# Performance work log

Measured on AMD Instinct MI355X. Metric: run time of the kernel, lower is better.

The kernel has to match this reference:

```python
import jax, jax.numpy as jnp
import numpy as np

N_BITS = 64
N_GROUPS = 8
P = N_BITS // N_GROUPS          # bits per group = 8
MAX_TABLE = 2 ** (P + N_GROUPS - 1)  # 32768, largest group-mapper table
BATCH = 524288


def setup_inputs() -> dict:
    key = jax.random.key(0)
    k1, k2, k3 = jax.random.split(key, 3)
    # input bit patterns [B, n_bits], values in {0,1}
    bits = jax.random.randint(k1, (BATCH, N_BITS), 0, 2, dtype=jnp.int32)
    # group mapper RAM tables, padded to max address space; table for group g
    # only uses the first 2^(P+g) addresses (addresses never exceed that range)
    group_tables = jax.random.uniform(k2, (N_GROUPS, P, MAX_TABLE), dtype=jnp.float32)
    # carry detector tables: one 1-neuron table per group boundary, binary outputs
    carry_tables = jax.random.randint(k3, (N_GROUPS - 1, 2 ** P), 0, 2, dtype=jnp.int32)
    return {"bits": bits, "group_tables": group_tables, "carry_tables": carry_tables}


def reference(bits, group_tables, carry_tables):
    B = bits.shape[0]
    gb = bits.reshape(B, N_GROUPS, P)                       # [B, G, P]
    # MSB-first address per group (matches reversed-bit enumeration in source)
    w = (2 ** (P - 1 - jnp.arange(P))).astype(jnp.int32)    # [P]
    gaddr = jnp.einsum('bgp,p->bg', gb, w)                  # [B, G] int32
    # carry detector g reads the raw bits of group g (independent of other carries)
    carries = carry_tables[jnp.arange(N_GROUPS - 1)[None, :],
                           gaddr[:, :N_GROUPS - 1]]          # [B, G-1] in {0,1}
    outs = []
    for g in range(N_GROUPS):  # small fixed loop over structurally distinct tables
        addr = gaddr[:, g]
        if g > 0:
            # mapper input = cat([group_bits, carries[0:g]]); group bits are high bits
            cw = (2 ** (g - 1 - jnp.arange(g))).astype(jnp.int32)
            addr = addr * (2 ** g) + carries[:, :g] @ cw
        # gather each neuron's table entry at this address -> [B, P]
        outs.append(jnp.take(group_tables[g], addr, axis=1).T)
    return jnp.stack(outs, axis=1).reshape(B, N_BITS)
```

## Files before the change

### kernel.cpp

```cpp
#include <hip/hip_runtime.h>

#define N_BITS   64
#define N_GROUPS 8
#define PDIM     8
#define MAX_TABLE 32768
#define BATCH    524288

__global__ __launch_bounds__(256) void comp_mapper_kernel(
    const int*   __restrict__ bits,
    const float* __restrict__ gt,
    const int*   __restrict__ ct,
    float*       __restrict__ out)
{
    const int tid = blockIdx.x * blockDim.x + threadIdx.x;
    const int g   = tid & 7;

    const int4* bp = reinterpret_cast<const int4*>(bits) + (size_t)tid * 2;
    int4 x = bp[0];
    int4 y = bp[1];

    int gaddr = (x.x << 7) | (x.y << 6) | (x.z << 5) | (x.w << 4)
              | (y.x << 3) | (y.y << 2) | (y.z << 1) |  y.w;

    int carry = 0;
    if (g < 7) carry = ct[g * 256 + gaddr];

    unsigned long long m = __ballot(carry);
    const int lane = threadIdx.x & 63;
    const int base = lane & ~7;
    unsigned f = (unsigned)((m >> base) & 0xFFull);
    unsigned v = (__brev(f) >> 24) >> (8 - g);

    const int addr = (gaddr << g) | (int)v;

    const float* t = gt + (size_t)g * (PDIM * MAX_TABLE) + addr;
    float4 o0, o1;
    o0.x = t[0 * MAX_TABLE];
    o0.y = t[1 * MAX_TABLE];
    o0.z = t[2 * MAX_TABLE];
    o0.w = t[3 * MAX_TABLE];
    o1.x = t[4 * MAX_TABLE];
    o1.y = t[5 * MAX_TABLE];
    o1.z = t[6 * MAX_TABLE];
    o1.w = t[7 * MAX_TABLE];

    float4* op = reinterpret_cast<float4*>(out) + (size_t)tid * 2;
    op[0] = o0;
    op[1] = o1;
}

extern "C" void kernel_launch(void* const* d_in, const int* in_sizes, int n_in,
                              void* d_out, int out_size, void* d_ws, size_t ws_size,
                              hipStream_t stream) {
    const int*   bits = (const int*)  d_in[0];
    const float* gt   = (const float*)d_in[1];
    const int*   ct   = (const int*)  d_in[2];
    float*       out  = (float*)      d_out;

    const int total_threads = BATCH * N_GROUPS;
    const int block = 256;
    const int grid  = total_threads / block;

    comp_mapper_kernel<<<grid, block, 0, stream>>>(bits, gt, ct, out);
}
```

Baseline: 321.3 us.

## Transpose group tables into workspace so each gather reads contiguous float4s

```diff
diff --git a/kernel.cpp b/kernel.cpp
--- a/kernel.cpp
+++ b/kernel.cpp
@@ -1,14 +1,34 @@
 #include <hip/hip_runtime.h>
 
-#define N_BITS   64
-#define N_GROUPS 8
-#define PDIM     8
+#define N_BITS    64
+#define N_GROUPS  8
+#define PDIM      8
 #define MAX_TABLE 32768
-#define BATCH    524288
+#define BATCH     524288
 
+__global__ __launch_bounds__(256) void transpose_tables(
+    const float* __restrict__ gt,
+    float*       __restrict__ tt)
+{
+    const int i  = blockIdx.x * blockDim.x + threadIdx.x;
+    const int a4 = i & (MAX_TABLE / 4 - 1);
+    const int gp = i >> 13;
+    const int p  = gp & 7;
+    const int g  = gp >> 3;
+
+    const float4 v = reinterpret_cast<const float4*>(gt)[i];
+    const int a = a4 * 4;
+    float* base = tt + (size_t)g * MAX_TABLE * PDIM + p;
+    base[(size_t)(a + 0) * PDIM] = v.x;
+    base[(size_t)(a + 1) * PDIM] = v.y;
+    base[(size_t)(a + 2) * PDIM] = v.z;
+    base[(size_t)(a + 3) * PDIM] = v.w;
+}
+
+template <bool TRANSPOSED>
 __global__ __launch_bounds__(256) void comp_mapper_kernel(
     const int*   __restrict__ bits,
-    const float* __restrict__ gt,
+    const float* __restrict__ tab,
     const int*   __restrict__ ct,
     float*       __restrict__ out)
 {
@@ -33,16 +53,19 @@
 
     const int addr = (gaddr << g) | (int)v;
 
-    const float* t = gt + (size_t)g * (PDIM * MAX_TABLE) + addr;
     float4 o0, o1;
-    o0.x = t[0 * MAX_TABLE];
-    o0.y = t[1 * MAX_TABLE];
-    o0.z = t[2 * MAX_TABLE];
-    o0.w = t[3 * MAX_TABLE];
-    o1.x = t[4 * MAX_TABLE];
-    o1.y = t[5 * MAX_TABLE];
-    o1.z = t[6 * MAX_TABLE];
-    o1.w = t[7 * MAX_TABLE];
+    if (TRANSPOSED) {
+        const float4* t = reinterpret_cast<const float4*>(
+            tab + ((size_t)g * MAX_TABLE + addr) * PDIM);
+        o0 = t[0];
+        o1 = t[1];
+    } else {
+        const float* t = tab + (size_t)g * (PDIM * MAX_TABLE) + addr;
+        o0.x = t[0 * MAX_TABLE]; o0.y = t[1 * MAX_TABLE];
+        o0.z = t[2 * MAX_TABLE]; o0.w = t[3 * MAX_TABLE];
+        o1.x = t[4 * MAX_TABLE]; o1.y = t[5 * MAX_TABLE];
+        o1.z = t[6 * MAX_TABLE]; o1.w = t[7 * MAX_TABLE];
+    }
 
     float4* op = reinterpret_cast<float4*>(out) + (size_t)tid * 2;
     op[0] = o0;
@@ -61,5 +84,14 @@
     const int block = 256;
     const int grid  = total_threads / block;
 
-    comp_mapper_kernel<<<grid, block, 0, stream>>>(bits, gt, ct, out);
+    const size_t tt_bytes = (size_t)N_GROUPS * MAX_TABLE * PDIM * sizeof(float);
+
+    if (ws_size >= tt_bytes) {
+        float* tt = (float*)d_ws;
+        const int t_threads = N_GROUPS * PDIM * MAX_TABLE / 4;
+        transpose_tables<<<t_threads / block, block, 0, stream>>>(gt, tt);
+        comp_mapper_kernel<true><<<grid, block, 0, stream>>>(bits, tt, ct, out);
+    } else {
+        comp_mapper_kernel<false><<<grid, block, 0, stream>>>(bits, gt, ct, out);
+    }
 }
```

Result: faster. 273.7 us (-14.8%).
